# Performance work log

Hardware: AMD Instinct MI355X
Metric: run time of the kernel (lower is better)

Reference implementation:

```python
import jax, jax.numpy as jnp
import numpy as np

N_NODES = 100000
N_EDGES = 1600000
HIDDEN = 128
OUT_DIM = 1
N_GRAPHS = 2048
VOCAB = 28  # atom types, Embedding(28, hidden_dim)


def setup_inputs() -> dict:
    key = jax.random.key(0)
    ks = jax.random.split(key, 14)
    s = 1.0 / np.sqrt(HIDDEN)
    inp = {
        "x_idx": jax.random.randint(ks[0], (N_NODES,), 0, VOCAB, dtype=jnp.int32),
        "edge_src": jax.random.randint(ks[1], (N_EDGES,), 0, N_NODES, dtype=jnp.int32),
        "edge_dst": jax.random.randint(ks[2], (N_EDGES,), 0, N_NODES, dtype=jnp.int32),
        "batch": jnp.sort(jax.random.randint(ks[3], (N_NODES,), 0, N_GRAPHS, dtype=jnp.int32)),
        # parameters
        "embed": jax.random.normal(ks[4], (VOCAB, HIDDEN), dtype=jnp.float32) * 0.02,
        "eps0": jnp.zeros((1,), dtype=jnp.float32),
        "w1_0": jax.random.normal(ks[5], (HIDDEN, HIDDEN), dtype=jnp.float32) * s,
        "b1_0": jnp.zeros((HIDDEN,), dtype=jnp.float32),
        "w2_0": jax.random.normal(ks[6], (HIDDEN, HIDDEN), dtype=jnp.float32) * s,
        "b2_0": jnp.zeros((HIDDEN,), dtype=jnp.float32),
        "eps1": jnp.zeros((1,), dtype=jnp.float32),
        "w1_1": jax.random.normal(ks[7], (HIDDEN, HIDDEN), dtype=jnp.float32) * s,
        "b1_1": jnp.zeros((HIDDEN,), dtype=jnp.float32),
        "w2_1": jax.random.normal(ks[8], (HIDDEN, OUT_DIM), dtype=jnp.float32) * s,
        "b2_1": jnp.zeros((OUT_DIM,), dtype=jnp.float32),
    }
    return inp


def _gin_layer(x, edge_src, edge_dst, eps, w1, b1, w2, b2):
    # A @ x via edge-list SpMM: out[dst] += x[src]  (same math as to_dense().matmul(x))
    agg = jax.ops.segment_sum(x[edge_src], edge_dst, num_segments=N_NODES)
    h = agg + (1.0 + eps) * x  # [N, in_feats]; eps broadcasts (shape [1])
    h = h @ w1 + b1            # linear1 (no nonlinearity between, as in source)
    return h @ w2 + b2         # linear2


def reference(x_idx, edge_src, edge_dst, batch, embed,
              eps0, w1_0, b1_0, w2_0, b2_0,
              eps1, w1_1, b1_1, w2_1, b2_1):
    x = embed[x_idx]  # [N, HIDDEN] — Embedding lookup (.squeeze(1) trivial here)
    x = jax.nn.relu(_gin_layer(x, edge_src, edge_dst, eps0, w1_0, b1_0, w2_0, b2_0))
    x = _gin_layer(x, edge_src, edge_dst, eps1, w1_1, b1_1, w2_1, b2_1)  # [N, 1]
    y_hat = jax.ops.segment_sum(x.squeeze(-1), batch, num_segments=N_GRAPHS)  # [G]
    return (y_hat, x)
```

## Files before the change

kernel.cpp:

```cpp
#include <hip/hip_runtime.h>

#define N_NODES  100000
#define N_EDGES  1600000
#define HIDDEN   128
#define N_GRAPHS 2048
#define VOCAB    28
#define NB       196
#define CAP      10000
#define EPB      6250
#define EPT      25
#define EWP      132
#define CSTR     29

__global__ void k_init(float* __restrict__ out, int* __restrict__ gcursor) {
    int i = blockIdx.x * blockDim.x + threadIdx.x;
    if (i < N_GRAPHS) out[i] = 0.0f;
    else if (i < N_GRAPHS + 256) gcursor[i - N_GRAPHS] = 0;
}

__global__ __launch_bounds__(256) void k_prep(const float* __restrict__ w1_0,
                                              const float* __restrict__ w2_0,
                                              const float* __restrict__ b1_0,
                                              const float* __restrict__ b2_0,
                                              const float* __restrict__ w1_1,
                                              const float* __restrict__ b1_1,
                                              const float* __restrict__ w2_1,
                                              const float* __restrict__ b2_1,
                                              float* __restrict__ Wc0,
                                              float* __restrict__ bc0,
                                              float* __restrict__ wc1,
                                              float* __restrict__ bc1) {
    int t = threadIdx.x;
    if (blockIdx.x < 64) {
        int g = blockIdx.x * 256 + t;
        int i = g >> 7, j = g & 127;
        float s = 0.f;
#pragma unroll 8
        for (int k = 0; k < HIDDEN; ++k)
            s += w1_0[i * HIDDEN + k] * w2_0[k * HIDDEN + j];
        Wc0[g] = s;
    } else {
        if (t < 128) {
            float s = 0.f;
#pragma unroll 8
            for (int k = 0; k < HIDDEN; ++k)
                s += b1_0[k] * w2_0[k * HIDDEN + t];
            bc0[t] = s + b2_0[t];
            if (t == 0) {
                float q = 0.f;
                for (int k = 0; k < HIDDEN; ++k) q += b1_1[k] * w2_1[k];
                bc1[0] = q + b2_1[0];
            }
        } else {
            int i = t - 128;
            float s = 0.f;
#pragma unroll 8
            for (int k = 0; k < HIDDEN; ++k)
                s += w1_1[i * HIDDEN + k] * w2_1[k];
            wc1[i] = s;
        }
    }
}

__global__ __launch_bounds__(256) void k_prep2(const float* __restrict__ embed,
                                               const float* __restrict__ Wc0,
                                               float* __restrict__ EW) {
    int g = blockIdx.x * 256 + threadIdx.x;
    if (g >= VOCAB * HIDDEN) return;
    int i = g >> 7, j = g & 127;
    float s = 0.f;
#pragma unroll 8
    for (int k = 0; k < HIDDEN; ++k)
        s += embed[i * HIDDEN + k] * Wc0[k * HIDDEN + j];
    EW[g] = s;
}

__global__ __launch_bounds__(256) void k_bin(const int* __restrict__ esrc,
                                             const int* __restrict__ edst,
                                             const int* __restrict__ x_idx,
                                             unsigned* __restrict__ binned,
                                             int* __restrict__ gcursor) {
    __shared__ int hist[256];
    __shared__ int scanbuf[256];
    __shared__ int lbase[256];
    __shared__ int lcur[256];
    __shared__ int gbase[256];
    __shared__ unsigned stage[EPB];
    __shared__ int tgt[EPB];

    const int tid = threadIdx.x;
    hist[tid] = 0;
    lcur[tid] = 0;
    __syncthreads();

    unsigned mypk[EPT];
    short    myb[EPT];
#pragma unroll
    for (int i = 0; i < EPT; ++i) {
        int idx = i * 256 + tid;
        myb[i] = -1;
        if (idx < EPB) {
            int e   = blockIdx.x * EPB + idx;
            int dst = edst[e];
            int src = esrc[e];
            int b   = dst >> 9;
            int dl  = dst & 511;
            int vix = x_idx[src];
            mypk[i] = ((unsigned)dl << 22) | ((unsigned)vix << 17) | (unsigned)src;
            myb[i]  = (short)b;
            atomicAdd(&hist[b], 1);
        }
    }
    __syncthreads();

    int v = hist[tid];
    scanbuf[tid] = v;
    __syncthreads();
    for (int off = 1; off < 256; off <<= 1) {
        int x = (tid >= off) ? scanbuf[tid - off] : 0;
        __syncthreads();
        scanbuf[tid] += x;
        __syncthreads();
    }
    lbase[tid] = scanbuf[tid] - v;
    if (tid < NB) gbase[tid] = (v > 0) ? atomicAdd(&gcursor[tid], v) : 0;
    __syncthreads();

#pragma unroll
    for (int i = 0; i < EPT; ++i) {
        if (myb[i] >= 0) {
            int b   = myb[i];
            int pos = lbase[b] + atomicAdd(&lcur[b], 1);
            stage[pos] = mypk[i];
            tgt[pos]   = b * CAP + gbase[b] + (pos - lbase[b]);
        }
    }
    __syncthreads();

    for (int i = tid; i < EPB; i += 256)
        binned[tgt[i]] = stage[i];
}

__global__ __launch_bounds__(256) void k_layerA(const unsigned* __restrict__ binned,
                                                const int* __restrict__ gcursor,
                                                const int* __restrict__ x_idx,
                                                const float* __restrict__ EW,
                                                const float* __restrict__ bc0,
                                                const float* __restrict__ wc1,
                                                const float* __restrict__ eps0,
                                                float* __restrict__ d) {
    __shared__ __align__(16) float ewp[VOCAB * EWP];
    __shared__ int lcnt[256 * CSTR];

    const int tid = threadIdx.x;
    const int b   = blockIdx.x >> 1;
    const int h   = blockIdx.x & 1;

    for (int i = tid; i < VOCAB * HIDDEN; i += 256) {
        int v = i >> 7, f = i & 127;
        ewp[v * EWP + f] = EW[i];
    }
    for (int i = tid; i < 256 * CSTR; i += 256) lcnt[i] = 0;
    __syncthreads();

    const int cnt = gcursor[b];
    const unsigned* bp = binned + (size_t)b * CAP;
    for (int i = tid; i < cnt; i += 256) {
        unsigned pk = bp[i];
        int dl = pk >> 22;
        if ((dl >> 8) == h)
            atomicAdd(&lcnt[(dl & 255) * CSTR + ((pk >> 17) & 31)], 1);
    }
    __syncthreads();

    const int nl = tid;
    const int n  = b * 512 + h * 256 + nl;

    float cf[VOCAB];
#pragma unroll
    for (int v = 0; v < VOCAB; ++v) cf[v] = (float)lcnt[nl * CSTR + v];

    const float s  = 1.0f + eps0[0];
    const int   xi = (n < N_NODES) ? x_idx[n] : 0;
    const float* exr = &ewp[xi * EWP];

    const float4* EW4 = reinterpret_cast<const float4*>(EW);
    const float4* b04 = reinterpret_cast<const float4*>(bc0);
    const float4* w14 = reinterpret_cast<const float4*>(wc1);

    float dacc = 0.f;
#pragma unroll 1
    for (int f4 = 0; f4 < 32; ++f4) {
        float4 a = b04[f4];
        float4 ex = *reinterpret_cast<const float4*>(exr + f4 * 4);
        a.x += s * ex.x; a.y += s * ex.y; a.z += s * ex.z; a.w += s * ex.w;
#pragma unroll
        for (int v = 0; v < VOCAB; ++v) {
            float4 e = EW4[v * 32 + f4];
            a.x += cf[v] * e.x;
            a.y += cf[v] * e.y;
            a.z += cf[v] * e.z;
            a.w += cf[v] * e.w;
        }
        float4 w = w14[f4];
        dacc += fmaxf(a.x, 0.f) * w.x + fmaxf(a.y, 0.f) * w.y
              + fmaxf(a.z, 0.f) * w.z + fmaxf(a.w, 0.f) * w.w;
    }
    if (n < N_NODES) d[n] = dacc;
}

__global__ __launch_bounds__(512) void k_B2(const unsigned* __restrict__ binned,
                                            const int* __restrict__ gcursor,
                                            const float* __restrict__ d,
                                            const int* __restrict__ batch,
                                            const float* __restrict__ eps1,
                                            const float* __restrict__ bc1,
                                            float* __restrict__ out) {
    __shared__ float racc[512];
    __shared__ float gacc[N_GRAPHS];

    const int tid = threadIdx.x;
    const int b   = blockIdx.x;
    const int n0  = b * 512;
    const int nlast = min(n0 + 511, N_NODES - 1);

    racc[tid] = 0.f;
    const int g0 = batch[n0];
    const int g1 = batch[nlast];
    for (int g = g0 + tid; g <= g1; g += 512) gacc[g] = 0.f;
    __syncthreads();

    const int cnt = gcursor[b];
    const unsigned* bp = binned + (size_t)b * CAP;
    for (int i = tid; i < cnt; i += 512) {
        unsigned pk = bp[i];
        atomicAdd(&racc[pk >> 22], d[pk & 0x1FFFFu]);
    }
    __syncthreads();

    int n = n0 + tid;
    if (n < N_NODES) {
        float r = (1.0f + eps1[0]) * d[n] + racc[tid] + bc1[0];
        out[N_GRAPHS + n] = r;
        atomicAdd(&gacc[batch[n]], r);
    }
    __syncthreads();
    for (int g = g0 + tid; g <= g1; g += 512) {
        float v = gacc[g];
        if (v != 0.f) atomicAdd(&out[g], v);
    }
}

extern "C" void kernel_launch(void* const* d_in, const int* in_sizes, int n_in,
                              void* d_out, int out_size, void* d_ws, size_t ws_size,
                              hipStream_t stream) {
    const int*   x_idx = (const int*)d_in[0];
    const int*   esrc  = (const int*)d_in[1];
    const int*   edst  = (const int*)d_in[2];
    const int*   batch = (const int*)d_in[3];
    const float* embed = (const float*)d_in[4];
    const float* eps0  = (const float*)d_in[5];
    const float* w1_0  = (const float*)d_in[6];
    const float* b1_0  = (const float*)d_in[7];
    const float* w2_0  = (const float*)d_in[8];
    const float* b2_0  = (const float*)d_in[9];
    const float* eps1  = (const float*)d_in[10];
    const float* w1_1  = (const float*)d_in[11];
    const float* b1_1  = (const float*)d_in[12];
    const float* w2_1  = (const float*)d_in[13];
    const float* b2_1  = (const float*)d_in[14];

    float* out = (float*)d_out;

    int*      gcursor = (int*)d_ws;
    unsigned* binned  = (unsigned*)(gcursor + 256);
    float*    d       = (float*)(binned + (size_t)NB * CAP);
    float*    Wc0     = d + N_NODES;
    float*    bc0     = Wc0 + HIDDEN * HIDDEN;
    float*    wc1     = bc0 + HIDDEN;
    float*    bc1     = wc1 + HIDDEN;
    float*    EW      = bc1 + 1;

    k_init<<<9, 256, 0, stream>>>(out, gcursor);

    k_prep<<<65, 256, 0, stream>>>(w1_0, w2_0, b1_0, b2_0, w1_1, b1_1, w2_1, b2_1,
                                   Wc0, bc0, wc1, bc1);
    k_prep2<<<(VOCAB * HIDDEN + 255) / 256, 256, 0, stream>>>(embed, Wc0, EW);

    k_bin<<<256, 256, 0, stream>>>(esrc, edst, x_idx, binned, gcursor);

    k_layerA<<<NB * 2, 256, 0, stream>>>(binned, gcursor, x_idx, EW, bc0, wc1, eps0, d);

    k_B2<<<NB, 512, 0, stream>>>(binned, gcursor, d, batch, eps1, bc1, out);
}
```

Baseline: 175.5 us.

## Replace edge binning with global-atomic count and aggregation sweeps

Drops the shared-memory bin/scatter kernel that packed edges by destination block. Layer 0 now builds a global per-vocab, per-node count matrix with global atomics. Layer 1 does a second edge sweep with global float atomics into an aggregate vector, and the final kernel reads that vector. This removes the binning pass and its shared-memory staging, but adds about 11 MB of zeroing, scattered global atomics over a large table, and one extra read of the edge list.

After: 288.1 us. 64.1% more time.

```diff
diff --git a/kernel.cpp b/kernel.cpp
--- a/kernel.cpp
+++ b/kernel.cpp
@@ -5,17 +5,18 @@
 #define HIDDEN   128
 #define N_GRAPHS 2048
 #define VOCAB    28
-#define NB       196
-#define CAP      10000
-#define EPB      6250
-#define EPT      25
-#define EWP      132
-#define CSTR     29
-
-__global__ void k_init(float* __restrict__ out, int* __restrict__ gcursor) {
-    int i = blockIdx.x * blockDim.x + threadIdx.x;
-    if (i < N_GRAPHS) out[i] = 0.0f;
-    else if (i < N_GRAPHS + 256) gcursor[i - N_GRAPHS] = 0;
+#define NPAD     100352
+
+__global__ __launch_bounds__(256) void k_zero(float* __restrict__ out,
+                                              int* __restrict__ ws) {
+    int i = blockIdx.x * 256 + threadIdx.x;
+    if (i < N_GRAPHS / 4) {
+        reinterpret_cast<int4*>(out)[i] = make_int4(0, 0, 0, 0);
+    }
+    int j = i - N_GRAPHS / 4;
+    if (j >= 0 && j < (VOCAB + 1) * NPAD / 4) {
+        reinterpret_cast<int4*>(ws)[j] = make_int4(0, 0, 0, 0);
+    }
 }
 
 __global__ __launch_bounds__(256) void k_prep(const float* __restrict__ w1_0,
@@ -75,114 +76,38 @@
     EW[g] = s;
 }
 
-__global__ __launch_bounds__(256) void k_bin(const int* __restrict__ esrc,
-                                             const int* __restrict__ edst,
-                                             const int* __restrict__ x_idx,
-                                             unsigned* __restrict__ binned,
-                                             int* __restrict__ gcursor) {
-    __shared__ int hist[256];
-    __shared__ int scanbuf[256];
-    __shared__ int lbase[256];
-    __shared__ int lcur[256];
-    __shared__ int gbase[256];
-    __shared__ unsigned stage[EPB];
-    __shared__ int tgt[EPB];
-
-    const int tid = threadIdx.x;
-    hist[tid] = 0;
-    lcur[tid] = 0;
-    __syncthreads();
-
-    unsigned mypk[EPT];
-    short    myb[EPT];
-#pragma unroll
-    for (int i = 0; i < EPT; ++i) {
-        int idx = i * 256 + tid;
-        myb[i] = -1;
-        if (idx < EPB) {
-            int e   = blockIdx.x * EPB + idx;
-            int dst = edst[e];
-            int src = esrc[e];
-            int b   = dst >> 9;
-            int dl  = dst & 511;
-            int vix = x_idx[src];
-            mypk[i] = ((unsigned)dl << 22) | ((unsigned)vix << 17) | (unsigned)src;
-            myb[i]  = (short)b;
-            atomicAdd(&hist[b], 1);
-        }
-    }
-    __syncthreads();
-
-    int v = hist[tid];
-    scanbuf[tid] = v;
-    __syncthreads();
-    for (int off = 1; off < 256; off <<= 1) {
-        int x = (tid >= off) ? scanbuf[tid - off] : 0;
-        __syncthreads();
-        scanbuf[tid] += x;
-        __syncthreads();
-    }
-    lbase[tid] = scanbuf[tid] - v;
-    if (tid < NB) gbase[tid] = (v > 0) ? atomicAdd(&gcursor[tid], v) : 0;
-    __syncthreads();
-
-#pragma unroll
-    for (int i = 0; i < EPT; ++i) {
-        if (myb[i] >= 0) {
-            int b   = myb[i];
-            int pos = lbase[b] + atomicAdd(&lcur[b], 1);
-            stage[pos] = mypk[i];
-            tgt[pos]   = b * CAP + gbase[b] + (pos - lbase[b]);
-        }
-    }
-    __syncthreads();
-
-    for (int i = tid; i < EPB; i += 256)
-        binned[tgt[i]] = stage[i];
-}
-
-__global__ __launch_bounds__(256) void k_layerA(const unsigned* __restrict__ binned,
-                                                const int* __restrict__ gcursor,
+__global__ __launch_bounds__(256) void k_sweep0(const int4* __restrict__ esrc4,
+                                                const int4* __restrict__ edst4,
+                                                const int* __restrict__ x_idx,
+                                                int* __restrict__ cnt) {
+    int i = blockIdx.x * 256 + threadIdx.x;
+    if (i >= N_EDGES / 4) return;
+    int4 s = esrc4[i];
+    int4 t = edst4[i];
+    atomicAdd(&cnt[x_idx[s.x] * NPAD + t.x], 1);
+    atomicAdd(&cnt[x_idx[s.y] * NPAD + t.y], 1);
+    atomicAdd(&cnt[x_idx[s.z] * NPAD + t.z], 1);
+    atomicAdd(&cnt[x_idx[s.w] * NPAD + t.w], 1);
+}
+
+__global__ __launch_bounds__(256) void k_layerA(const int* __restrict__ cnt,
                                                 const int* __restrict__ x_idx,
                                                 const float* __restrict__ EW,
                                                 const float* __restrict__ bc0,
                                                 const float* __restrict__ wc1,
                                                 const float* __restrict__ eps0,
                                                 float* __restrict__ d) {
-    __shared__ __align__(16) float ewp[VOCAB * EWP];
-    __shared__ int lcnt[256 * CSTR];
-
-    const int tid = threadIdx.x;
-    const int b   = blockIdx.x >> 1;
-    const int h   = blockIdx.x & 1;
-
-    for (int i = tid; i < VOCAB * HIDDEN; i += 256) {
-        int v = i >> 7, f = i & 127;
-        ewp[v * EWP + f] = EW[i];
-    }
-    for (int i = tid; i < 256 * CSTR; i += 256) lcnt[i] = 0;
-    __syncthreads();
-
-    const int cnt = gcursor[b];
-    const unsigned* bp = binned + (size_t)b * CAP;
-    for (int i = tid; i < cnt; i += 256) {
-        unsigned pk = bp[i];
-        int dl = pk >> 22;
-        if ((dl >> 8) == h)
-            atomicAdd(&lcnt[(dl & 255) * CSTR + ((pk >> 17) & 31)], 1);
-    }
-    __syncthreads();
-
-    const int nl = tid;
-    const int n  = b * 512 + h * 256 + nl;
+    const int n = blockIdx.x * 256 + threadIdx.x;
+    const bool valid = (n < N_NODES);
+    const int xi = valid ? x_idx[n] : 0;
+    const float s = 1.0f + eps0[0];
 
     float cf[VOCAB];
 #pragma unroll
-    for (int v = 0; v < VOCAB; ++v) cf[v] = (float)lcnt[nl * CSTR + v];
-
-    const float s  = 1.0f + eps0[0];
-    const int   xi = (n < N_NODES) ? x_idx[n] : 0;
-    const float* exr = &ewp[xi * EWP];
+    for (int v = 0; v < VOCAB; ++v) {
+        float c = (float)cnt[v * NPAD + n];
+        cf[v] = c + ((v == xi) ? s : 0.0f);
+    }
 
     const float4* EW4 = reinterpret_cast<const float4*>(EW);
     const float4* b04 = reinterpret_cast<const float4*>(bc0);
@@ -192,8 +117,6 @@
 #pragma unroll 1
     for (int f4 = 0; f4 < 32; ++f4) {
         float4 a = b04[f4];
-        float4 ex = *reinterpret_cast<const float4*>(exr + f4 * 4);
-        a.x += s * ex.x; a.y += s * ex.y; a.z += s * ex.z; a.w += s * ex.w;
 #pragma unroll
         for (int v = 0; v < VOCAB; ++v) {
             float4 e = EW4[v * 32 + f4];
@@ -206,41 +129,41 @@
         dacc += fmaxf(a.x, 0.f) * w.x + fmaxf(a.y, 0.f) * w.y
               + fmaxf(a.z, 0.f) * w.z + fmaxf(a.w, 0.f) * w.w;
     }
-    if (n < N_NODES) d[n] = dacc;
-}
-
-__global__ __launch_bounds__(512) void k_B2(const unsigned* __restrict__ binned,
-                                            const int* __restrict__ gcursor,
-                                            const float* __restrict__ d,
-                                            const int* __restrict__ batch,
-                                            const float* __restrict__ eps1,
-                                            const float* __restrict__ bc1,
-                                            float* __restrict__ out) {
-    __shared__ float racc[512];
+    if (valid) d[n] = dacc;
+}
+
+__global__ __launch_bounds__(256) void k_sweep1(const int4* __restrict__ esrc4,
+                                                const int4* __restrict__ edst4,
+                                                const float* __restrict__ d,
+                                                float* __restrict__ agg) {
+    int i = blockIdx.x * 256 + threadIdx.x;
+    if (i >= N_EDGES / 4) return;
+    int4 s = esrc4[i];
+    int4 t = edst4[i];
+    atomicAdd(&agg[t.x], d[s.x]);
+    atomicAdd(&agg[t.y], d[s.y]);
+    atomicAdd(&agg[t.z], d[s.z]);
+    atomicAdd(&agg[t.w], d[s.w]);
+}
+
+__global__ __launch_bounds__(512) void k_final(const float* __restrict__ dvec,
+                                               const float* __restrict__ agg,
+                                               const int* __restrict__ batch,
+                                               const float* __restrict__ eps1,
+                                               const float* __restrict__ bc1,
+                                               float* __restrict__ out) {
     __shared__ float gacc[N_GRAPHS];
-
     const int tid = threadIdx.x;
-    const int b   = blockIdx.x;
-    const int n0  = b * 512;
+    const int n0 = blockIdx.x * 512;
     const int nlast = min(n0 + 511, N_NODES - 1);
-
-    racc[tid] = 0.f;
     const int g0 = batch[n0];
     const int g1 = batch[nlast];
     for (int g = g0 + tid; g <= g1; g += 512) gacc[g] = 0.f;
     __syncthreads();
 
-    const int cnt = gcursor[b];
-    const unsigned* bp = binned + (size_t)b * CAP;
-    for (int i = tid; i < cnt; i += 512) {
-        unsigned pk = bp[i];
-        atomicAdd(&racc[pk >> 22], d[pk & 0x1FFFFu]);
-    }
-    __syncthreads();
-
     int n = n0 + tid;
     if (n < N_NODES) {
-        float r = (1.0f + eps1[0]) * d[n] + racc[tid] + bc1[0];
+        float r = (1.0f + eps1[0]) * dvec[n] + agg[n] + bc1[0];
         out[N_GRAPHS + n] = r;
         atomicAdd(&gacc[batch[n]], r);
     }
@@ -272,24 +195,28 @@
 
     float* out = (float*)d_out;
 
-    int*      gcursor = (int*)d_ws;
-    unsigned* binned  = (unsigned*)(gcursor + 256);
-    float*    d       = (float*)(binned + (size_t)NB * CAP);
-    float*    Wc0     = d + N_NODES;
-    float*    bc0     = Wc0 + HIDDEN * HIDDEN;
-    float*    wc1     = bc0 + HIDDEN;
-    float*    bc1     = wc1 + HIDDEN;
-    float*    EW      = bc1 + 1;
-
-    k_init<<<9, 256, 0, stream>>>(out, gcursor);
+    int*   cnt = (int*)d_ws;
+    float* agg = (float*)(cnt + VOCAB * NPAD);
+    float* d   = agg + NPAD;
+    float* Wc0 = d + N_NODES;
+    float* bc0 = Wc0 + HIDDEN * HIDDEN;
+    float* wc1 = bc0 + HIDDEN;
+    float* bc1 = wc1 + HIDDEN;
+    float* EW  = bc1 + 1;
+
+    k_zero<<<2844, 256, 0, stream>>>(out, cnt);
 
     k_prep<<<65, 256, 0, stream>>>(w1_0, w2_0, b1_0, b2_0, w1_1, b1_1, w2_1, b2_1,
                                    Wc0, bc0, wc1, bc1);
     k_prep2<<<(VOCAB * HIDDEN + 255) / 256, 256, 0, stream>>>(embed, Wc0, EW);
 
-    k_bin<<<256, 256, 0, stream>>>(esrc, edst, x_idx, binned, gcursor);
-
-    k_layerA<<<NB * 2, 256, 0, stream>>>(binned, gcursor, x_idx, EW, bc0, wc1, eps0, d);
-
-    k_B2<<<NB, 512, 0, stream>>>(binned, gcursor, d, batch, eps1, bc1, out);
-}
+    k_sweep0<<<(N_EDGES / 4 + 255) / 256, 256, 0, stream>>>(
+        (const int4*)esrc, (const int4*)edst, x_idx, cnt);
+
+    k_layerA<<<NPAD / 256, 256, 0, stream>>>(cnt, x_idx, EW, bc0, wc1, eps0, d);
+
+    k_sweep1<<<(N_EDGES / 4 + 255) / 256, 256, 0, stream>>>(
+        (const int4*)esrc, (const int4*)edst, d, agg);
+
+    k_final<<<NPAD / 512, 512, 0, stream>>>(d, agg, batch, eps1, bc1, out);
+}
```

## Fuse weight prep into binning kernel and halve node bins to 256

Applied to the files above, without the earlier changes.

Folds the weight-precompute work into the edge-binning launch as extra blocks, and reassociates the embedding product as (embed·W1)·W2, so there is no full 128x128 Wc0 product and one fewer launch. Bins shrink to 256 destination nodes, so layer-A blocks no longer filter half their bin. The self term is folded into the count coefficients, which removes the per-node shared EW copy. The cost is more bins and blocks, 512-thread binning with a larger scan, and a wider k_B2 grid with an early-exit guard.

After: 168.9 us. -3.8%, faster.

```diff
diff --git a/kernel.cpp b/kernel.cpp
--- a/kernel.cpp
+++ b/kernel.cpp
@@ -5,90 +5,82 @@
 #define HIDDEN   128
 #define N_GRAPHS 2048
 #define VOCAB    28
-#define NB       196
-#define CAP      10000
-#define EPB      6250
-#define EPT      25
-#define EWP      132
+#define NB       392
+#define CAP      5000
+#define NBIN     512
+#define EPB      3125
+#define EPT      7
 #define CSTR     29
 
-__global__ void k_init(float* __restrict__ out, int* __restrict__ gcursor) {
-    int i = blockIdx.x * blockDim.x + threadIdx.x;
+__global__ __launch_bounds__(256) void k_init(float* __restrict__ out,
+                                              int* __restrict__ gcursor) {
+    int i = blockIdx.x * 256 + threadIdx.x;
     if (i < N_GRAPHS) out[i] = 0.0f;
-    else if (i < N_GRAPHS + 256) gcursor[i - N_GRAPHS] = 0;
-}
-
-__global__ __launch_bounds__(256) void k_prep(const float* __restrict__ w1_0,
-                                              const float* __restrict__ w2_0,
-                                              const float* __restrict__ b1_0,
-                                              const float* __restrict__ b2_0,
-                                              const float* __restrict__ w1_1,
-                                              const float* __restrict__ b1_1,
-                                              const float* __restrict__ w2_1,
-                                              const float* __restrict__ b2_1,
-                                              float* __restrict__ Wc0,
-                                              float* __restrict__ bc0,
-                                              float* __restrict__ wc1,
-                                              float* __restrict__ bc1) {
-    int t = threadIdx.x;
-    if (blockIdx.x < 64) {
-        int g = blockIdx.x * 256 + t;
-        int i = g >> 7, j = g & 127;
-        float s = 0.f;
-#pragma unroll 8
-        for (int k = 0; k < HIDDEN; ++k)
-            s += w1_0[i * HIDDEN + k] * w2_0[k * HIDDEN + j];
-        Wc0[g] = s;
-    } else {
-        if (t < 128) {
+    else if (i < N_GRAPHS + NB) gcursor[i - N_GRAPHS] = 0;
+}
+
+__global__ __launch_bounds__(512) void k_binprep(const int* __restrict__ esrc,
+                                                 const int* __restrict__ edst,
+                                                 const int* __restrict__ x_idx,
+                                                 unsigned* __restrict__ binned,
+                                                 int* __restrict__ gcursor,
+                                                 const float* __restrict__ embed,
+                                                 const float* __restrict__ w1_0,
+                                                 const float* __restrict__ w2_0,
+                                                 const float* __restrict__ b1_0,
+                                                 const float* __restrict__ b2_0,
+                                                 const float* __restrict__ w1_1,
+                                                 const float* __restrict__ b1_1,
+                                                 const float* __restrict__ w2_1,
+                                                 const float* __restrict__ b2_1,
+                                                 float* __restrict__ T,
+                                                 float* __restrict__ bc0,
+                                                 float* __restrict__ wc1,
+                                                 float* __restrict__ bc1) {
+    const int tid = threadIdx.x;
+    const int bid = blockIdx.x;
+
+    if (bid >= NBIN) {
+        if (bid < NBIN + 7) {
+            int g = (bid - NBIN) * 512 + tid;
+            int i = g >> 7, j = g & 127;
             float s = 0.f;
 #pragma unroll 8
             for (int k = 0; k < HIDDEN; ++k)
-                s += b1_0[k] * w2_0[k * HIDDEN + t];
-            bc0[t] = s + b2_0[t];
-            if (t == 0) {
-                float q = 0.f;
-                for (int k = 0; k < HIDDEN; ++k) q += b1_1[k] * w2_1[k];
-                bc1[0] = q + b2_1[0];
+                s += embed[i * HIDDEN + k] * w1_0[k * HIDDEN + j];
+            T[g] = s;
+        } else {
+            if (tid < 128) {
+                float s = 0.f;
+#pragma unroll 8
+                for (int k = 0; k < HIDDEN; ++k)
+                    s += b1_0[k] * w2_0[k * HIDDEN + tid];
+                bc0[tid] = s + b2_0[tid];
+                if (tid == 0) {
+                    float q = 0.f;
+                    for (int k = 0; k < HIDDEN; ++k) q += b1_1[k] * w2_1[k];
+                    bc1[0] = q + b2_1[0];
+                }
+            } else if (tid < 256) {
+                int i = tid - 128;
+                float s = 0.f;
+#pragma unroll 8
+                for (int k = 0; k < HIDDEN; ++k)
+                    s += w1_1[i * HIDDEN + k] * w2_1[k];
+                wc1[i] = s;
             }
-        } else {
-            int i = t - 128;
-            float s = 0.f;
-#pragma unroll 8
-            for (int k = 0; k < HIDDEN; ++k)
-                s += w1_1[i * HIDDEN + k] * w2_1[k];
-            wc1[i] = s;
-        }
-    }
-}
-
-__global__ __launch_bounds__(256) void k_prep2(const float* __restrict__ embed,
-                                               const float* __restrict__ Wc0,
-                                               float* __restrict__ EW) {
-    int g = blockIdx.x * 256 + threadIdx.x;
-    if (g >= VOCAB * HIDDEN) return;
-    int i = g >> 7, j = g & 127;
-    float s = 0.f;
-#pragma unroll 8
-    for (int k = 0; k < HIDDEN; ++k)
-        s += embed[i * HIDDEN + k] * Wc0[k * HIDDEN + j];
-    EW[g] = s;
-}
-
-__global__ __launch_bounds__(256) void k_bin(const int* __restrict__ esrc,
-                                             const int* __restrict__ edst,
-                                             const int* __restrict__ x_idx,
-                                             unsigned* __restrict__ binned,
-                                             int* __restrict__ gcursor) {
-    __shared__ int hist[256];
-    __shared__ int scanbuf[256];
-    __shared__ int lbase[256];
-    __shared__ int lcur[256];
-    __shared__ int gbase[256];
+        }
+        return;
+    }
+
+    __shared__ int hist[512];
+    __shared__ int scanbuf[512];
+    __shared__ int lbase[512];
+    __shared__ int lcur[512];
+    __shared__ int gbase[512];
     __shared__ unsigned stage[EPB];
     __shared__ int tgt[EPB];
 
-    const int tid = threadIdx.x;
     hist[tid] = 0;
     lcur[tid] = 0;
     __syncthreads();
@@ -97,14 +89,14 @@
     short    myb[EPT];
 #pragma unroll
     for (int i = 0; i < EPT; ++i) {
-        int idx = i * 256 + tid;
+        int idx = i * 512 + tid;
         myb[i] = -1;
         if (idx < EPB) {
-            int e   = blockIdx.x * EPB + idx;
+            int e   = bid * EPB + idx;
             int dst = edst[e];
             int src = esrc[e];
-            int b   = dst >> 9;
-            int dl  = dst & 511;
+            int b   = dst >> 8;
+            int dl  = dst & 255;
             int vix = x_idx[src];
             mypk[i] = ((unsigned)dl << 22) | ((unsigned)vix << 17) | (unsigned)src;
             myb[i]  = (short)b;
@@ -116,7 +108,7 @@
     int v = hist[tid];
     scanbuf[tid] = v;
     __syncthreads();
-    for (int off = 1; off < 256; off <<= 1) {
+    for (int off = 1; off < 512; off <<= 1) {
         int x = (tid >= off) ? scanbuf[tid - off] : 0;
         __syncthreads();
         scanbuf[tid] += x;
@@ -132,16 +124,32 @@
             int b   = myb[i];
             int pos = lbase[b] + atomicAdd(&lcur[b], 1);
             stage[pos] = mypk[i];
-            tgt[pos]   = b * CAP + gbase[b] + (pos - lbase[b]);
-        }
-    }
-    __syncthreads();
-
-    for (int i = tid; i < EPB; i += 256)
-        binned[tgt[i]] = stage[i];
-}
-
-__global__ __launch_bounds__(256) void k_layerA(const unsigned* __restrict__ binned,
+            tgt[pos]   = (b << 12) | (pos - lbase[b]);
+        }
+    }
+    __syncthreads();
+
+    for (int i = tid; i < EPB; i += 512) {
+        int u = tgt[i];
+        int b = u >> 12, lr = u & 4095;
+        binned[b * CAP + gbase[b] + lr] = stage[i];
+    }
+}
+
+__global__ __launch_bounds__(512) void k_prep2(const float* __restrict__ T,
+                                               const float* __restrict__ w2_0,
+                                               float* __restrict__ EW) {
+    int g = blockIdx.x * 512 + threadIdx.x;
+    if (g >= VOCAB * HIDDEN) return;
+    int i = g >> 7, j = g & 127;
+    float s = 0.f;
+#pragma unroll 8
+    for (int k = 0; k < HIDDEN; ++k)
+        s += T[i * HIDDEN + k] * w2_0[k * HIDDEN + j];
+    EW[g] = s;
+}
+
+__global__ __launch_bounds__(256) void k_layerC(const unsigned* __restrict__ binned,
                                                 const int* __restrict__ gcursor,
                                                 const int* __restrict__ x_idx,
                                                 const float* __restrict__ EW,
@@ -149,17 +157,11 @@
                                                 const float* __restrict__ wc1,
                                                 const float* __restrict__ eps0,
                                                 float* __restrict__ d) {
-    __shared__ __align__(16) float ewp[VOCAB * EWP];
     __shared__ int lcnt[256 * CSTR];
 
     const int tid = threadIdx.x;
-    const int b   = blockIdx.x >> 1;
-    const int h   = blockIdx.x & 1;
-
-    for (int i = tid; i < VOCAB * HIDDEN; i += 256) {
-        int v = i >> 7, f = i & 127;
-        ewp[v * EWP + f] = EW[i];
-    }
+    const int b   = blockIdx.x;
+
     for (int i = tid; i < 256 * CSTR; i += 256) lcnt[i] = 0;
     __syncthreads();
 
@@ -167,22 +169,19 @@
     const unsigned* bp = binned + (size_t)b * CAP;
     for (int i = tid; i < cnt; i += 256) {
         unsigned pk = bp[i];
-        int dl = pk >> 22;
-        if ((dl >> 8) == h)
-            atomicAdd(&lcnt[(dl & 255) * CSTR + ((pk >> 17) & 31)], 1);
-    }
-    __syncthreads();
-
-    const int nl = tid;
-    const int n  = b * 512 + h * 256 + nl;
+        atomicAdd(&lcnt[(pk >> 22) * CSTR + ((pk >> 17) & 31)], 1);
+    }
+    __syncthreads();
+
+    const int n      = b * 256 + tid;
+    const bool valid = (n < N_NODES);
+    const int xi     = valid ? x_idx[n] : 0;
+    const float s    = 1.0f + eps0[0];
 
     float cf[VOCAB];
 #pragma unroll
-    for (int v = 0; v < VOCAB; ++v) cf[v] = (float)lcnt[nl * CSTR + v];
-
-    const float s  = 1.0f + eps0[0];
-    const int   xi = (n < N_NODES) ? x_idx[n] : 0;
-    const float* exr = &ewp[xi * EWP];
+    for (int v = 0; v < VOCAB; ++v)
+        cf[v] = (float)lcnt[tid * CSTR + v] + ((v == xi) ? s : 0.0f);
 
     const float4* EW4 = reinterpret_cast<const float4*>(EW);
     const float4* b04 = reinterpret_cast<const float4*>(bc0);
@@ -192,8 +191,6 @@
 #pragma unroll 1
     for (int f4 = 0; f4 < 32; ++f4) {
         float4 a = b04[f4];
-        float4 ex = *reinterpret_cast<const float4*>(exr + f4 * 4);
-        a.x += s * ex.x; a.y += s * ex.y; a.z += s * ex.z; a.w += s * ex.w;
 #pragma unroll
         for (int v = 0; v < VOCAB; ++v) {
             float4 e = EW4[v * 32 + f4];
@@ -206,33 +203,34 @@
         dacc += fmaxf(a.x, 0.f) * w.x + fmaxf(a.y, 0.f) * w.y
               + fmaxf(a.z, 0.f) * w.z + fmaxf(a.w, 0.f) * w.w;
     }
-    if (n < N_NODES) d[n] = dacc;
-}
-
-__global__ __launch_bounds__(512) void k_B2(const unsigned* __restrict__ binned,
+    if (valid) d[n] = dacc;
+}
+
+__global__ __launch_bounds__(256) void k_B2(const unsigned* __restrict__ binned,
                                             const int* __restrict__ gcursor,
                                             const float* __restrict__ d,
                                             const int* __restrict__ batch,
                                             const float* __restrict__ eps1,
                                             const float* __restrict__ bc1,
                                             float* __restrict__ out) {
-    __shared__ float racc[512];
+    __shared__ float racc[256];
     __shared__ float gacc[N_GRAPHS];
 
     const int tid = threadIdx.x;
     const int b   = blockIdx.x;
-    const int n0  = b * 512;
-    const int nlast = min(n0 + 511, N_NODES - 1);
+    const int n0  = b * 256;
+    if (n0 >= N_NODES) return;
+    const int nlast = min(n0 + 255, N_NODES - 1);
 
     racc[tid] = 0.f;
     const int g0 = batch[n0];
     const int g1 = batch[nlast];
-    for (int g = g0 + tid; g <= g1; g += 512) gacc[g] = 0.f;
+    for (int g = g0 + tid; g <= g1; g += 256) gacc[g] = 0.f;
     __syncthreads();
 
     const int cnt = gcursor[b];
     const unsigned* bp = binned + (size_t)b * CAP;
-    for (int i = tid; i < cnt; i += 512) {
+    for (int i = tid; i < cnt; i += 256) {
         unsigned pk = bp[i];
         atomicAdd(&racc[pk >> 22], d[pk & 0x1FFFFu]);
     }
@@ -245,7 +243,7 @@
         atomicAdd(&gacc[batch[n]], r);
     }
     __syncthreads();
-    for (int g = g0 + tid; g <= g1; g += 512) {
+    for (int g = g0 + tid; g <= g1; g += 256) {
         float v = gacc[g];
         if (v != 0.f) atomicAdd(&out[g], v);
     }
@@ -273,23 +271,24 @@
     float* out = (float*)d_out;
 
     int*      gcursor = (int*)d_ws;
-    unsigned* binned  = (unsigned*)(gcursor + 256);
+    unsigned* binned  = (unsigned*)(gcursor + 512);
     float*    d       = (float*)(binned + (size_t)NB * CAP);
-    float*    Wc0     = d + N_NODES;
-    float*    bc0     = Wc0 + HIDDEN * HIDDEN;
+    float*    T       = d + 100352;
+    float*    bc0     = T + VOCAB * HIDDEN;
     float*    wc1     = bc0 + HIDDEN;
     float*    bc1     = wc1 + HIDDEN;
     float*    EW      = bc1 + 1;
 
-    k_init<<<9, 256, 0, stream>>>(out, gcursor);
-
-    k_prep<<<65, 256, 0, stream>>>(w1_0, w2_0, b1_0, b2_0, w1_1, b1_1, w2_1, b2_1,
-                                   Wc0, bc0, wc1, bc1);
-    k_prep2<<<(VOCAB * HIDDEN + 255) / 256, 256, 0, stream>>>(embed, Wc0, EW);
-
-    k_bin<<<256, 256, 0, stream>>>(esrc, edst, x_idx, binned, gcursor);
-
-    k_layerA<<<NB * 2, 256, 0, stream>>>(binned, gcursor, x_idx, EW, bc0, wc1, eps0, d);
-
-    k_B2<<<NB, 512, 0, stream>>>(binned, gcursor, d, batch, eps1, bc1, out);
-}
+    k_init<<<(N_GRAPHS + NB + 255) / 256, 256, 0, stream>>>(out, gcursor);
+
+    k_binprep<<<NBIN + 8, 512, 0, stream>>>(esrc, edst, x_idx, binned, gcursor,
+                                            embed, w1_0, w2_0, b1_0, b2_0,
+                                            w1_1, b1_1, w2_1, b2_1,
+                                            T, bc0, wc1, bc1);
+
+    k_prep2<<<7, 512, 0, stream>>>(T, w2_0, EW);
+
+    k_layerC<<<NB, 256, 0, stream>>>(binned, gcursor, x_idx, EW, bc0, wc1, eps0, d);
+
+    k_B2<<<NB, 256, 0, stream>>>(binned, gcursor, d, batch, eps1, bc1, out);
+}
```
